# Kernel tuning notes

Hardware: AMD Instinct MI355X
Metric: run time of the kernel (lower is better)

Reference implementation:

```python
import jax, jax.numpy as jnp
import numpy as np
from jax import lax

SCALE = 1.0
SHIFT = 0.0
H = 1024
IN = 1024
B = 64
S = 512


def setup_inputs() -> dict:
    key = jax.random.key(0)
    ks = jax.random.split(key, 9)
    s_in = 1.0 / np.sqrt(IN)
    s_h = 1.0 / np.sqrt(H)
    return {
        "x": jax.random.normal(ks[0], (B, S, IN), jnp.float32),
        # layer 0: ih Linear(IN, 4H), hh Linear(H, 4H) — torch stores W as [out, in]
        "W_ih0": jax.random.uniform(ks[1], (4 * H, IN), jnp.float32, -s_in, s_in),
        "b_ih0": jax.random.uniform(ks[2], (4 * H,), jnp.float32, -s_in, s_in),
        "W_hh0": jax.random.uniform(ks[3], (4 * H, H), jnp.float32, -s_h, s_h),
        "b_hh0": jax.random.uniform(ks[4], (4 * H,), jnp.float32, -s_h, s_h),
        # layer 1: ih Linear(H, 4H), hh Linear(H, 4H)
        "W_ih1": jax.random.uniform(ks[5], (4 * H, H), jnp.float32, -s_h, s_h),
        "b_ih1": jax.random.uniform(ks[6], (4 * H,), jnp.float32, -s_h, s_h),
        "W_hh1": jax.random.uniform(ks[7], (4 * H, H), jnp.float32, -s_h, s_h),
        "b_hh1": jax.random.uniform(ks[8], (4 * H,), jnp.float32, -s_h, s_h),
    }


def _scaled_sigmoid(x):
    return SCALE * jax.nn.sigmoid(x) + SHIFT


def _lstm_layer(x_seq, W_ih, b_ih, W_hh, b_hh):
    """x_seq: (B, S, D). Returns (outputs (B,S,H), h_n (B,H), c_n (B,H))."""
    b = x_seq.shape[0]
    # precompute input projections for all timesteps: (S, B, 4H)
    xp = (jnp.einsum('bsd,gd->sbg', x_seq, W_ih) + b_ih).astype(x_seq.dtype)

    def step(carry, xp_t):
        h, c = carry
        gates = xp_t + h @ W_hh.T + b_hh  # (B, 4H)
        i_g, f_g, g_g, o_g = jnp.split(gates, 4, axis=-1)
        i = _scaled_sigmoid(i_g)
        f = _scaled_sigmoid(f_g)
        g = jnp.tanh(g_g)
        o = _scaled_sigmoid(o_g)
        c_next = f * c + i * g
        h_next = o * jnp.tanh(c_next)
        return (h_next, c_next), h_next

    h0 = jnp.zeros((b, W_hh.shape[1]), x_seq.dtype)
    c0 = jnp.zeros((b, W_hh.shape[1]), x_seq.dtype)
    (h_n, c_n), ys = lax.scan(step, (h0, c0), xp)
    return ys.transpose(1, 0, 2), h_n, c_n


def reference(x, W_ih0, b_ih0, W_hh0, b_hh0, W_ih1, b_ih1, W_hh1, b_hh1):
    out0, h0, c0 = _lstm_layer(x, W_ih0, b_ih0, W_hh0, b_hh0)
    out1, h1, c1 = _lstm_layer(out0, W_ih1, b_ih1, W_hh1, b_hh1)
    h_n = jnp.stack([h0, h1], axis=0)  # (num_layers, B, H)
    c_n = jnp.stack([c0, c1], axis=0)
    return out1, h_n, c_n
```

## Files before the change

### kernel.cpp

```cpp
#include <hip/hip_runtime.h>
#include <stdint.h>

typedef __attribute__((ext_vector_type(8))) short short8;
typedef __attribute__((ext_vector_type(4))) float f32x4;

#define MFMA16(a, b, c) __builtin_amdgcn_mfma_f32_16x16x32_bf16((a), (b), (c), 0, 0, 0)
#define AL(p) __hip_atomic_load((p), __ATOMIC_RELAXED, __HIP_MEMORY_SCOPE_AGENT)
#define AS(p, v) __hip_atomic_store((p), (v), __ATOMIC_RELAXED, __HIP_MEMORY_SCOPE_AGENT)

__device__ __forceinline__ unsigned short f2bf(float f) {
  unsigned u = __float_as_uint(f);
  u = (u + 0x7FFFu + ((u >> 16) & 1u)) >> 16;
  return (unsigned short)u;
}
__device__ __forceinline__ float bf2f(unsigned short u) {
  return __uint_as_float(((unsigned)u) << 16);
}

__global__ void k_prep(const float* __restrict__ x,
                       const float* __restrict__ w0, const float* __restrict__ w1,
                       const float* __restrict__ w2, const float* __restrict__ w3,
                       const float* __restrict__ a0, const float* __restrict__ b0,
                       const float* __restrict__ a1, const float* __restrict__ b1,
                       unsigned short* __restrict__ xbf,
                       unsigned short* __restrict__ wbf,
                       float* __restrict__ bias0, float* __restrict__ bias1) {
  const int gid = blockIdx.x * blockDim.x + threadIdx.x;
  const int stride = gridDim.x * blockDim.x;
  for (int i = gid; i < 8192; i += stride) {
    if (i < 4096) bias0[i] = a0[i] + b0[i];
    else          bias1[i - 4096] = a1[i - 4096] + b1[i - 4096];
  }
  for (int i = gid; i < 8388608; i += stride) {
    float4 v = reinterpret_cast<const float4*>(x)[i];
    ushort4 o;
    o.x = f2bf(v.x); o.y = f2bf(v.y); o.z = f2bf(v.z); o.w = f2bf(v.w);
    reinterpret_cast<ushort4*>(xbf)[i] = o;
  }
  for (int i = gid; i < 4194304; i += stride) {
    const float* sp = (i < 1048576) ? w0 : (i < 2097152) ? w1
                     : (i < 3145728) ? w2 : w3;
    float4 v = reinterpret_cast<const float4*>(sp)[i & 1048575];
    ushort4 o;
    o.x = f2bf(v.x); o.y = f2bf(v.y); o.z = f2bf(v.z); o.w = f2bf(v.w);
    reinterpret_cast<ushort4*>(wbf)[i] = o;
  }
}

__global__ __launch_bounds__(256) void k_gemm(
    const unsigned short* __restrict__ A,
    const unsigned short* __restrict__ W,
    const float* __restrict__ bias,
    unsigned short* __restrict__ out,
    int mode) {
  const int tid = threadIdx.x, l = tid & 63, wv = tid >> 6;
  const int wm = wv >> 1, wn = wv & 1;
  const int bid = blockIdx.x;
  const int swz = ((bid & 7) << 10) + (bid >> 3);
  const int tm = swz & 255, tn = swz >> 8;
  const int m_base = tm * 128 + wm * 64;
  const int n_base = tn * 128 + wn * 64;
  const int lr = l & 15, k8 = (l >> 4) << 3;

  size_t a_off[4], b_off[4];
#pragma unroll
  for (int i = 0; i < 4; ++i) {
    int r = m_base + i * 16 + lr;
    int ar = mode ? r : (((r & 63) << 9) + (r >> 6));
    a_off[i] = ((size_t)ar << 10) + k8;
    int nr = n_base + i * 16 + lr;
    b_off[i] = ((size_t)nr << 10) + k8;
  }
  f32x4 acc[4][4] = {};
#pragma unroll 2
  for (int k0 = 0; k0 < 1024; k0 += 32) {
    short8 a[4], b[4];
#pragma unroll
    for (int i = 0; i < 4; ++i) a[i] = *reinterpret_cast<const short8*>(A + a_off[i] + k0);
#pragma unroll
    for (int j = 0; j < 4; ++j) b[j] = *reinterpret_cast<const short8*>(W + b_off[j] + k0);
#pragma unroll
    for (int i = 0; i < 4; ++i)
#pragma unroll
      for (int j = 0; j < 4; ++j) acc[i][j] = MFMA16(a[i], b[j], acc[i][j]);
  }
  const int oq = (l >> 4) << 2, oc = l & 15;
#pragma unroll
  for (int j = 0; j < 4; ++j) {
    int col = n_base + j * 16 + oc;
    int gate = col >> 10, jc = col & 1023;
    size_t cidx = (size_t)((jc << 2) + gate);
    float bs = bias[col];
#pragma unroll
    for (int i = 0; i < 4; ++i) {
      int r0 = m_base + i * 16 + oq;
#pragma unroll
      for (int q = 0; q < 4; ++q)
        out[(((size_t)(r0 + q)) << 12) + cidx] = f2bf(acc[i][j][q] + bs);
    }
  }
}

__device__ __forceinline__ void gemm_chunk(
    const unsigned short* __restrict__ out0,
    const unsigned short* __restrict__ Wih1,
    const float* __restrict__ bias1,
    unsigned short* __restrict__ xb,
    char* smem, int g, int hc0, int c,
    int tid, int l, int ks, int lr16, int k8) {
  const int cg = (ks << 4) + lr16;
  const int gate = cg >> 5, jl = cg & 31;
  const int wrow = (gate << 10) + hc0 + jl;
  const float bsv = bias1[wrow];
  unsigned short* trs = (unsigned short*)smem;

  for (int mb = 0; mb < 16; ++mb) {
    f32x4 acc[4] = {{0.f,0.f,0.f,0.f},{0.f,0.f,0.f,0.f},{0.f,0.f,0.f,0.f},{0.f,0.f,0.f,0.f}};
#pragma unroll 1
    for (int kh = 0; kh < 2; ++kh) {
      short8 st[8];
#pragma unroll
      for (int s = 0; s < 8; ++s) {
        int ch = tid + (s << 9);
        int row = ch >> 6, kc = ch & 63;
        int t = (c << 6) + (mb << 2) + (row >> 4);
        int b = (g << 4) + (row & 15);
        st[s] = *reinterpret_cast<const short8*>(
            out0 + (((size_t)((t << 6) + b)) << 10) + (kh << 9) + (kc << 3));
      }
#pragma unroll
      for (int s = 0; s < 8; ++s) {
        int ch = tid + (s << 9);
        int row = ch >> 6, kc = ch & 63;
        *reinterpret_cast<short8*>(smem + (row << 10) + ((kc ^ (row & 7)) << 4)) = st[s];
      }
      __syncthreads();
#pragma unroll
      for (int kk = 0; kk < 16; ++kk) {
        short8 bfr = *reinterpret_cast<const short8*>(
            Wih1 + ((size_t)wrow << 10) + (kh << 9) + (kk << 5) + k8);
        int kc = (kk << 2) + (k8 >> 3);
#pragma unroll
        for (int mt = 0; mt < 4; ++mt) {
          int row = (mt << 4) + lr16;
          short8 a = *reinterpret_cast<const short8*>(
              smem + (row << 10) + ((kc ^ (row & 7)) << 4));
          acc[mt] = MFMA16(a, bfr, acc[mt]);
        }
      }
      __syncthreads();
    }
#pragma unroll
    for (int mt = 0; mt < 4; ++mt)
#pragma unroll
      for (int q = 0; q < 4; ++q) {
        int bi = ((l >> 4) << 2) + q;
        trs[(((mt << 4) + bi) << 7) + (jl << 2) + gate] = f2bf(acc[mt][q] + bsv);
      }
    __syncthreads();
#pragma unroll
    for (int s = 0; s < 2; ++s) {
      int ch = (tid << 1) + s;
      short8 v = *reinterpret_cast<const short8*>(trs + (ch << 3));
      unsigned short* dst = xb + (mb << 13) + (ch << 3);
      asm volatile("global_store_dwordx4 %0, %1, off sc0 sc1"
                   :: "v"(dst), "v"(v) : "memory");
    }
    __syncthreads();
  }
  asm volatile("s_waitcnt vmcnt(0)" ::: "memory");
  __syncthreads();
}

__device__ __forceinline__ void rec0_body(
    const unsigned short* __restrict__ xp,
    const unsigned short* __restrict__ Whh,
    unsigned short* __restrict__ hbuf,
    int* __restrict__ gflags,
    unsigned short* __restrict__ out_bf,
    float* __restrict__ hn, float* __restrict__ cn,
    const unsigned short* __restrict__ Wih1,
    const float* __restrict__ bias1,
    unsigned short* __restrict__ xpp_partner,
    const int* __restrict__ pflag1,
    int* __restrict__ fx_self,
    float* part, int w, int g) {
  const int tid = threadIdx.x;
  const int l = tid & 63, ks = tid >> 6;
  const int hc0 = w << 5;
  const int lr16 = l & 15, k8 = (l >> 4) << 3;

  short8 bf[8][4];
#pragma unroll
  for (int nn = 0; nn < 8; ++nn) {
    const int c_wg = (nn << 4) + lr16;
    const unsigned short* wp =
        Whh + ((size_t)(((c_wg >> 5) << 10) + hc0 + (c_wg & 31)) << 10) + (ks << 7) + k8;
#pragma unroll
    for (int kk = 0; kk < 4; ++kk)
      bf[nn][kk] = *reinterpret_cast<const short8*>(wp + (kk << 5));
  }

  const int arow = (g << 4) + lr16;
  const size_t aoff = ((size_t)arow << 10) + (ks << 7) + k8;

  const int b_l = tid >> 5;
  const int j = tid & 31;
  const int b_g = (g << 4) + b_l;
  const int hcol = hc0 + j;

  float cs = 0.f;

  auto xload = [&](int t) -> uint2 {
    return *reinterpret_cast<const uint2*>(
        xp + (((size_t)((t << 6) + b_g)) << 12) + (hcol << 2));
  };

  auto step = [&](int t, uint2 xv) {
    if (t > 0) {
      const unsigned short* ab = hbuf + ((size_t)(t & 1) << 16) + aoff;
      short8 av[4];
#pragma unroll
      for (int kk = 0; kk < 4; ++kk) {
        const unsigned short* p = ab + (kk << 5);
        asm volatile("global_load_dwordx4 %0, %1, off sc0 sc1"
                     : "=v"(av[kk]) : "v"(p) : "memory");
      }
      asm volatile("s_waitcnt vmcnt(0)" ::: "memory");
      __builtin_amdgcn_sched_barrier(0);
      f32x4 acc[8] = {{0.f,0.f,0.f,0.f},{0.f,0.f,0.f,0.f},{0.f,0.f,0.f,0.f},{0.f,0.f,0.f,0.f},
                      {0.f,0.f,0.f,0.f},{0.f,0.f,0.f,0.f},{0.f,0.f,0.f,0.f},{0.f,0.f,0.f,0.f}};
#pragma unroll
      for (int kk = 0; kk < 4; ++kk)
#pragma unroll
        for (int nn = 0; nn < 8; ++nn)
          acc[nn] = MFMA16(av[kk], bf[nn][kk], acc[nn]);
#pragma unroll
      for (int nn = 0; nn < 8; ++nn)
#pragma unroll
        for (int q = 0; q < 4; ++q) {
          int bq = ((l >> 4) << 2) + q;
          part[(((ks << 4) + bq) << 7) + (nn << 4) + lr16] = acc[nn][q];
        }
    }
    __syncthreads();

    float hv, cv;
    unsigned short h16;
    {
      float gi = bf2f((unsigned short)(xv.x)), gf = bf2f((unsigned short)(xv.x >> 16));
      float gg = bf2f((unsigned short)(xv.y)), go = bf2f((unsigned short)(xv.y >> 16));
      if (t > 0) {
        float si = 0.f, sf = 0.f, sg = 0.f, so = 0.f;
#pragma unroll
        for (int ksx = 0; ksx < 8; ++ksx) {
          const float* p = part + (((ksx << 4) + b_l) << 7) + j;
          si += p[0]; sf += p[32]; sg += p[64]; so += p[96];
        }
        gi += si; gf += sf; gg += sg; go += so;
      }
      float iv = 1.f / (1.f + __expf(-gi));
      float fv = 1.f / (1.f + __expf(-gf));
      float gv = tanhf(gg);
      float ov = 1.f / (1.f + __expf(-go));
      cs = fv * cs + iv * gv;
      hv = ov * tanhf(cs);
      cv = cs;
      h16 = f2bf(hv);
      AS(hbuf + ((size_t)((t + 1) & 1) << 16) + ((size_t)b_g << 10) + hcol, h16);
    }
    asm volatile("s_waitcnt vmcnt(0)" ::: "memory");
    __syncthreads();
    if (tid == 0) AS(&gflags[w], t + 1);

    AS(out_bf + ((((size_t)t << 6) + b_g) << 10) + hcol, h16);
    if (t == 511) {
      hn[((size_t)b_g << 10) + hcol] = hv;
      cn[((size_t)b_g << 10) + hcol] = cv;
    } else {
      const int base = ks << 2;
      for (;;) {
        int f = (l < 4) ? AL(&gflags[base + l]) : 0x7fffffff;
        if (__all(f > t)) break;
        __builtin_amdgcn_s_sleep(1);
      }
    }
  };

  uint2 zz = {0u, 0u};
  uint2 xA[4] = {zz, zz, zz, zz}, xB[4] = {zz, zz, zz, zz};
#pragma unroll
  for (int s = 0; s < 4; ++s) xA[s] = xload(s);
  for (int tc = 0; tc < 512; tc += 8) {
#pragma unroll
    for (int s = 0; s < 4; ++s) xB[s] = xload(tc + 4 + s);
#pragma unroll
    for (int s = 0; s < 4; ++s) step(tc + s, xA[s]);
    if (tc + 8 < 512) {
#pragma unroll
      for (int s = 0; s < 4; ++s) xA[s] = xload(tc + 8 + s);
    }
#pragma unroll
    for (int s = 0; s < 4; ++s) step(tc + 4 + s, xB[s]);
  }

  asm volatile("s_waitcnt vmcnt(0)" ::: "memory");
  __syncthreads();
  if (tid == 0) AS(&gflags[w], 1000);

  if (tid == 0) {
    for (;;) {
      bool ok = true;
      for (int i = 0; i < 32; ++i)
        if (AL(&gflags[i]) < 1000) { ok = false; break; }
      if (ok) break;
      __builtin_amdgcn_s_sleep(16);
    }
  }
  __syncthreads();
  for (int c = 5; c < 8; ++c) {
    const int need = (c - 1) << 6;
    if (tid == 0) {
      while (AL(pflag1) < need) __builtin_amdgcn_s_sleep(16);
    }
    __syncthreads();
    gemm_chunk(out_bf, Wih1, bias1,
               xpp_partner + ((size_t)(c & 1) << 17),
               (char*)part, g, hc0, c, tid, l, ks, lr16, k8);
    if (tid == 0) AS(fx_self, c + 1);
  }
}

__device__ __forceinline__ void layer1_body(
    const unsigned short* __restrict__ out0,
    const unsigned short* __restrict__ Wih1,
    const float* __restrict__ bias1,
    const unsigned short* __restrict__ Whh1,
    unsigned short* __restrict__ xpp,
    unsigned short* __restrict__ hbuf,
    int* __restrict__ gflags0,
    int* __restrict__ gflags1,
    const int* __restrict__ fx_self,
    float* __restrict__ outf,
    float* __restrict__ hn, float* __restrict__ cn,
    float* part, int u, int g) {
  const int tid = threadIdx.x;
  const int l = tid & 63, ks = tid >> 6;
  const int hc0 = u << 5;
  const int lr16 = l & 15, k8 = (l >> 4) << 3;

  short8 bf[8][4];
#pragma unroll
  for (int nn = 0; nn < 8; ++nn) {
    const int c_wg = (nn << 4) + lr16;
    const unsigned short* wp =
        Whh1 + ((size_t)(((c_wg >> 5) << 10) + hc0 + (c_wg & 31)) << 10) + (ks << 7) + k8;
#pragma unroll
    for (int kk = 0; kk < 4; ++kk)
      bf[nn][kk] = *reinterpret_cast<const short8*>(wp + (kk << 5));
  }

  const int arow = (g << 4) + lr16;
  const size_t aoff = ((size_t)arow << 10) + (ks << 7) + k8;
  const int b_l = tid >> 5, j = tid & 31;
  const int b_g = (g << 4) + b_l;
  const int hcol = hc0 + j;

  float cs = 0.f;

  for (int c = 0; c < 8; ++c) {
    if (c < 5) {
      const int thr = ((c + 1) << 6) + 1;
      if (tid == 0) {
        for (;;) {
          bool ok = true;
          for (int i = 0; i < 32; ++i)
            if (AL(&gflags0[i]) < thr) { ok = false; break; }
          if (ok) break;
          __builtin_amdgcn_s_sleep(16);
        }
      }
      __syncthreads();
      gemm_chunk(out0, Wih1, bias1,
                 xpp + ((size_t)(c & 1) << 17),
                 (char*)part, g, hc0, c, tid, l, ks, lr16, k8);
    } else {
      if (tid == 0) {
        while (AL(fx_self) < c + 1) __builtin_amdgcn_s_sleep(16);
      }
      __syncthreads();
    }

    const unsigned short* xb = xpp + ((size_t)(c & 1) << 17);
    for (int ti = 0; ti < 64; ++ti) {
      const int t = (c << 6) + ti;
      uint2 xv;
      {
        const unsigned short* p = xb + (((ti << 4) + b_l) << 7) + (j << 2);
        asm volatile("global_load_dwordx2 %0, %1, off sc0 sc1"
                     : "=v"(xv) : "v"(p) : "memory");
      }

      if (t > 0) {
        const unsigned short* ab = hbuf + ((size_t)(t & 1) << 16) + aoff;
        short8 av[4];
#pragma unroll
        for (int kk = 0; kk < 4; ++kk) {
          const unsigned short* p = ab + (kk << 5);
          asm volatile("global_load_dwordx4 %0, %1, off sc0 sc1"
                       : "=v"(av[kk]) : "v"(p) : "memory");
        }
        asm volatile("s_waitcnt vmcnt(0)" ::: "memory");
        __builtin_amdgcn_sched_barrier(0);
        f32x4 acc[8] = {{0.f,0.f,0.f,0.f},{0.f,0.f,0.f,0.f},{0.f,0.f,0.f,0.f},{0.f,0.f,0.f,0.f},
                        {0.f,0.f,0.f,0.f},{0.f,0.f,0.f,0.f},{0.f,0.f,0.f,0.f},{0.f,0.f,0.f,0.f}};
#pragma unroll
        for (int kk = 0; kk < 4; ++kk)
#pragma unroll
          for (int nn = 0; nn < 8; ++nn)
            acc[nn] = MFMA16(av[kk], bf[nn][kk], acc[nn]);
#pragma unroll
        for (int nn = 0; nn < 8; ++nn)
#pragma unroll
          for (int q = 0; q < 4; ++q) {
            int bq = ((l >> 4) << 2) + q;
            part[(((ks << 4) + bq) << 7) + (nn << 4) + lr16] = acc[nn][q];
          }
      } else {
        asm volatile("s_waitcnt vmcnt(0)" ::: "memory");
      }
      __syncthreads();

      float hv, cv;
      unsigned short h16;
      {
        float gi = bf2f((unsigned short)(xv.x)), gf = bf2f((unsigned short)(xv.x >> 16));
        float gg = bf2f((unsigned short)(xv.y)), go = bf2f((unsigned short)(xv.y >> 16));
        if (t > 0) {
          float si = 0.f, sf = 0.f, sg = 0.f, so = 0.f;
#pragma unroll
          for (int ksx = 0; ksx < 8; ++ksx) {
            const float* p = part + (((ksx << 4) + b_l) << 7) + j;
            si += p[0]; sf += p[32]; sg += p[64]; so += p[96];
          }
          gi += si; gf += sf; gg += sg; go += so;
        }
        float iv = 1.f / (1.f + __expf(-gi));
        float fv = 1.f / (1.f + __expf(-gf));
        float gv = tanhf(gg);
        float ov = 1.f / (1.f + __expf(-go));
        cs = fv * cs + iv * gv;
        hv = ov * tanhf(cs);
        cv = cs;
        h16 = f2bf(hv);
        AS(hbuf + ((size_t)((t + 1) & 1) << 16) + ((size_t)b_g << 10) + hcol, h16);
      }
      asm volatile("s_waitcnt vmcnt(0)" ::: "memory");
      __syncthreads();
      if (tid == 0) AS(&gflags1[u], t + 1);

      outf[((((size_t)b_g << 9) + t) << 10) + hcol] = hv;
      if (t == 511) {
        hn[((size_t)b_g << 10) + hcol] = hv;
        cn[((size_t)b_g << 10) + hcol] = cv;
      } else {
        const int base = ks << 2;
        for (;;) {
          int f = (l < 4) ? AL(&gflags1[base + l]) : 0x7fffffff;
          if (__all(f > t)) break;
          __builtin_amdgcn_s_sleep(1);
        }
      }
    }
  }
}

__global__ __launch_bounds__(512, 2) void k_fused(
    const unsigned short* __restrict__ xp0,
    const unsigned short* __restrict__ Whh0,
    unsigned short* __restrict__ hb0,
    int* __restrict__ flags0,
    unsigned short* __restrict__ out0,
    float* __restrict__ hn, float* __restrict__ cn,
    const unsigned short* __restrict__ Wih1,
    const float* __restrict__ bias1,
    const unsigned short* __restrict__ Whh1,
    unsigned short* __restrict__ xpp_all,
    unsigned short* __restrict__ hb1,
    int* __restrict__ flags1,
    int* __restrict__ fx,
    float* __restrict__ outf) {
  __shared__ float part[8 * 16 * 128];
  const int wg = blockIdx.x;
  if (wg < 128) {
    rec0_body(xp0, Whh0, hb0, flags0 + ((wg >> 5) << 8), out0, hn, cn,
              Wih1, bias1,
              xpp_all + ((size_t)wg << 18),
              &flags1[((wg >> 5) << 8) + (wg & 31)],
              &fx[wg],
              part, wg & 31, wg >> 5);
  } else {
    const int w1 = wg - 128;
    layer1_body(out0, Wih1, bias1, Whh1,
                xpp_all + ((size_t)w1 << 18),
                hb1, flags0 + ((w1 >> 5) << 8), flags1 + ((w1 >> 5) << 8),
                &fx[w1],
                outf, hn + 65536, cn + 65536,
                part, w1 & 31, w1 >> 5);
  }
}

extern "C" void kernel_launch(void* const* d_in, const int* in_sizes, int n_in,
                              void* d_out, int out_size, void* d_ws, size_t ws_size,
                              hipStream_t stream) {
  (void)in_sizes; (void)n_in; (void)out_size; (void)ws_size;
  const float* x    = (const float*)d_in[0];
  const float* Wih0 = (const float*)d_in[1];
  const float* bih0 = (const float*)d_in[2];
  const float* Whh0 = (const float*)d_in[3];
  const float* bhh0 = (const float*)d_in[4];
  const float* Wih1 = (const float*)d_in[5];
  const float* bih1 = (const float*)d_in[6];
  const float* Whh1 = (const float*)d_in[7];
  const float* bhh1 = (const float*)d_in[8];
  float* dout = (float*)d_out;

  char* ws = (char*)d_ws;
  int*            flags0 = (int*)ws;
  int*            flags1 = (int*)(ws + 4096);
  int*            fx     = (int*)(ws + 8192);
  unsigned short* hb0    = (unsigned short*)(ws + 12288);
  unsigned short* hb1    = (unsigned short*)(ws + 274432);
  float*          bias0  = (float*)(ws + 536576);
  float*          bias1  = (float*)(ws + 552960);
  unsigned short* wbf    = (unsigned short*)(ws + 569344);
  unsigned short* xbf    = wbf + 16777216;
  unsigned short* out0   = xbf + 33554432;
  unsigned short* xpb    = out0 + 33554432;

  hipMemsetAsync(flags0, 0, 12288, stream);

  k_prep<<<2048, 256, 0, stream>>>(x, Wih0, Whh0, Wih1, Whh1,
                                   bih0, bhh0, bih1, bhh1,
                                   xbf, wbf, bias0, bias1);

  float* hn = dout + 33554432;
  float* cn = dout + 33554432 + 131072;

  k_gemm<<<8192, 256, 0, stream>>>(xbf, wbf + 0, bias0, xpb, 0);

  k_fused<<<256, 512, 0, stream>>>(xpb, wbf + 4194304, hb0, flags0,
                                   out0, hn, cn,
                                   wbf + 8388608, bias1, wbf + 12582912,
                                   xbf, hb1, flags1, fx, dout);
}
```

Baseline: 4.394 ms.

## Wait on layer-0 progress per sub-block inside gemm_chunk instead of per chunk

```diff
diff --git a/kernel.cpp b/kernel.cpp
--- a/kernel.cpp
+++ b/kernel.cpp
@@ -55,9 +55,7 @@
     int mode) {
   const int tid = threadIdx.x, l = tid & 63, wv = tid >> 6;
   const int wm = wv >> 1, wn = wv & 1;
-  const int bid = blockIdx.x;
-  const int swz = ((bid & 7) << 10) + (bid >> 3);
-  const int tm = swz & 255, tn = swz >> 8;
+  const int tm = blockIdx.x >> 5, tn = blockIdx.x & 31;
   const int m_base = tm * 128 + wm * 64;
   const int n_base = tn * 128 + wn * 64;
   const int lr = l & 15, k8 = (l >> 4) << 3;
@@ -106,6 +104,8 @@
     const unsigned short* __restrict__ Wih1,
     const float* __restrict__ bias1,
     unsigned short* __restrict__ xb,
+    const int* __restrict__ gf0,
+    int* __restrict__ gmin_lds,
     char* smem, int g, int hc0, int c,
     int tid, int l, int ks, int lr16, int k8) {
   const int cg = (ks << 4) + lr16;
@@ -114,7 +114,24 @@
   const float bsv = bias1[wrow];
   unsigned short* trs = (unsigned short*)smem;
 
+  int gmin = 0;
   for (int mb = 0; mb < 16; ++mb) {
+    const int thr = (c << 6) + (mb << 2) + 5;
+    if (gmin < thr) {
+      if (tid == 0) {
+        int m;
+        for (;;) {
+          m = 0x7fffffff;
+          for (int i = 0; i < 32; ++i) { int f = AL(&gf0[i]); m = (f < m) ? f : m; }
+          if (m >= thr) break;
+          __builtin_amdgcn_s_sleep(4);
+        }
+        *gmin_lds = m;
+      }
+      __syncthreads();
+      gmin = *gmin_lds;
+    }
+
     f32x4 acc[4] = {{0.f,0.f,0.f,0.f},{0.f,0.f,0.f,0.f},{0.f,0.f,0.f,0.f},{0.f,0.f,0.f,0.f}};
 #pragma unroll 1
     for (int kh = 0; kh < 2; ++kh) {
@@ -184,7 +201,7 @@
     unsigned short* __restrict__ xpp_partner,
     const int* __restrict__ pflag1,
     int* __restrict__ fx_self,
-    float* part, int w, int g) {
+    float* part, int* gmin_lds, int w, int g) {
   const int tid = threadIdx.x;
   const int l = tid & 63, ks = tid >> 6;
   const int hc0 = w << 5;
@@ -326,6 +343,7 @@
     __syncthreads();
     gemm_chunk(out_bf, Wih1, bias1,
                xpp_partner + ((size_t)(c & 1) << 17),
+               gflags, gmin_lds,
                (char*)part, g, hc0, c, tid, l, ks, lr16, k8);
     if (tid == 0) AS(fx_self, c + 1);
   }
@@ -343,7 +361,7 @@
     const int* __restrict__ fx_self,
     float* __restrict__ outf,
     float* __restrict__ hn, float* __restrict__ cn,
-    float* part, int u, int g) {
+    float* part, int* gmin_lds, int u, int g) {
   const int tid = threadIdx.x;
   const int l = tid & 63, ks = tid >> 6;
   const int hc0 = u << 5;
@@ -370,19 +388,9 @@
 
   for (int c = 0; c < 8; ++c) {
     if (c < 5) {
-      const int thr = ((c + 1) << 6) + 1;
-      if (tid == 0) {
-        for (;;) {
-          bool ok = true;
-          for (int i = 0; i < 32; ++i)
-            if (AL(&gflags0[i]) < thr) { ok = false; break; }
-          if (ok) break;
-          __builtin_amdgcn_s_sleep(16);
-        }
-      }
-      __syncthreads();
       gemm_chunk(out0, Wih1, bias1,
                  xpp + ((size_t)(c & 1) << 17),
+                 gflags0, gmin_lds,
                  (char*)part, g, hc0, c, tid, l, ks, lr16, k8);
     } else {
       if (tid == 0) {
@@ -491,6 +499,7 @@
     int* __restrict__ fx,
     float* __restrict__ outf) {
   __shared__ float part[8 * 16 * 128];
+  __shared__ int gmin;
   const int wg = blockIdx.x;
   if (wg < 128) {
     rec0_body(xp0, Whh0, hb0, flags0 + ((wg >> 5) << 8), out0, hn, cn,
@@ -498,7 +507,7 @@
               xpp_all + ((size_t)wg << 18),
               &flags1[((wg >> 5) << 8) + (wg & 31)],
               &fx[wg],
-              part, wg & 31, wg >> 5);
+              part, &gmin, wg & 31, wg >> 5);
   } else {
     const int w1 = wg - 128;
     layer1_body(out0, Wih1, bias1, Whh1,
@@ -506,7 +515,7 @@
                 hb1, flags0 + ((w1 >> 5) << 8), flags1 + ((w1 >> 5) << 8),
                 &fx[w1],
                 outf, hn + 65536, cn + 65536,
-                part, w1 & 31, w1 >> 5);
+                part, &gmin, w1 & 31, w1 >> 5);
   }
 }
 
```

Measured after the change: 4.063 ms. -7.5%, faster.
